# Optimization experiments

Measured on AMD Instinct MI355X. Metric: run time of the kernel, lower is better.

Reference implementation:

```python
import jax, jax.numpy as jnp
import numpy as np

B, D_IN, H, D_OUT, K = 8192, 2048, 2048, 1024, 4
LOGVAR_INIT = -5.0


def setup_inputs() -> dict:
    key = jax.random.key(0)
    ks = jax.random.split(key, 32)
    dims = [(D_IN, H), (H, H), (H, D_OUT)]
    inp = {"x": jax.random.normal(ks[0], (B, D_IN), dtype=jnp.float32)}
    i = 1
    for l, (din, dout) in enumerate(dims):
        inp[f"w_mu{l}"] = 0.1 * jax.random.normal(ks[i], (K, dout, din), dtype=jnp.float32); i += 1
        inp[f"b_mu{l}"] = 0.1 * jax.random.normal(ks[i], (K, dout), dtype=jnp.float32); i += 1
        inp[f"w_lv{l}"] = jnp.full((K,), LOGVAR_INIT, dtype=jnp.float32)
        inp[f"b_lv{l}"] = jnp.full((K,), LOGVAR_INIT, dtype=jnp.float32)
        inp[f"ml{l}"] = jnp.zeros((K,), dtype=jnp.float32)
        # reparameterization noise (randn_like in the torch code), one per component
        inp[f"w_n{l}"] = jax.random.normal(ks[i], (K, dout, din), dtype=jnp.float32); i += 1
        inp[f"b_n{l}"] = jax.random.normal(ks[i], (K, dout), dtype=jnp.float32); i += 1
    return inp


def _mixture_linear(x, w_mu, b_mu, w_lv, b_lv, ml, w_n, b_n):
    # n_components <= n_samples: all K components used, weighted by softmax(mix_logits)
    mix_w = jax.nn.softmax(ml)                               # [K]
    w = w_mu + jnp.exp(0.5 * w_lv)[:, None, None] * w_n      # [K, O, I]
    b = b_mu + jnp.exp(0.5 * b_lv)[:, None] * b_n            # [K, O]
    # sum_k mix_w[k] * (x @ w[k].T + b[k])
    out = jnp.einsum('bi,koi,k->bo', x, w, mix_w)
    out = out + jnp.einsum('k,ko->o', mix_w, b)
    return out


def reference(x,
              w_mu0, b_mu0, w_lv0, b_lv0, ml0, w_n0, b_n0,
              w_mu1, b_mu1, w_lv1, b_lv1, ml1, w_n1, b_n1,
              w_mu2, b_mu2, w_lv2, b_lv2, ml2, w_n2, b_n2):
    h = jax.nn.relu(_mixture_linear(x, w_mu0, b_mu0, w_lv0, b_lv0, ml0, w_n0, b_n0))
    h = jax.nn.relu(_mixture_linear(h, w_mu1, b_mu1, w_lv1, b_lv1, ml1, w_n1, b_n1))
    h = _mixture_linear(h, w_mu2, b_mu2, w_lv2, b_lv2, ml2, w_n2, b_n2)
    return jax.nn.softmax(h, axis=1)
```

## Files before the change

kernel.cpp:

```cpp
#include <hip/hip_runtime.h>
#include <hip/hip_fp16.h>

typedef _Float16 half8 __attribute__((ext_vector_type(8)));
typedef _Float16 half4 __attribute__((ext_vector_type(4)));
typedef float floatx4 __attribute__((ext_vector_type(4)));

#define GLDS16(g, l)                                                           \
  __builtin_amdgcn_global_load_lds(                                            \
      (const __attribute__((address_space(1))) void*)(g),                      \
      (__attribute__((address_space(3))) void*)(l), 16, 0, 0)

__device__ inline void mix_coeffs(const float* lv, const float* ml,
                                  float* cmu, float* cn) {
  float m0 = ml[0], m1 = ml[1], m2 = ml[2], m3 = ml[3];
  float mx = fmaxf(fmaxf(m0, m1), fmaxf(m2, m3));
  float e0 = __expf(m0 - mx), e1 = __expf(m1 - mx);
  float e2 = __expf(m2 - mx), e3 = __expf(m3 - mx);
  float inv = 1.0f / (e0 + e1 + e2 + e3);
  cmu[0] = e0 * inv; cmu[1] = e1 * inv; cmu[2] = e2 * inv; cmu[3] = e3 * inv;
  cn[0] = cmu[0] * __expf(0.5f * lv[0]);
  cn[1] = cmu[1] * __expf(0.5f * lv[1]);
  cn[2] = cmu[2] * __expf(0.5f * lv[2]);
  cn[3] = cmu[3] * __expf(0.5f * lv[3]);
}

__global__ __launch_bounds__(256) void prep_w(
    const float* __restrict__ mu, const float* __restrict__ nz,
    const float* __restrict__ lv, const float* __restrict__ ml,
    _Float16* __restrict__ out, int count) {
  float cmu[4], cn[4];
  mix_coeffs(lv, ml, cmu, cn);
  long i = ((long)blockIdx.x * 256 + threadIdx.x) * 4;
  if (i >= count) return;
  float rx = 0.f, ry = 0.f, rz = 0.f, rw = 0.f;
#pragma unroll
  for (int k = 0; k < 4; ++k) {
    float4 a = *(const float4*)(mu + (long)k * count + i);
    float4 b = *(const float4*)(nz + (long)k * count + i);
    rx += cmu[k] * a.x + cn[k] * b.x;
    ry += cmu[k] * a.y + cn[k] * b.y;
    rz += cmu[k] * a.z + cn[k] * b.z;
    rw += cmu[k] * a.w + cn[k] * b.w;
  }
  half4 h = {(_Float16)rx, (_Float16)ry, (_Float16)rz, (_Float16)rw};
  *(half4*)(out + i) = h;
}

__global__ __launch_bounds__(256) void prep_b(
    const float* __restrict__ bmu, const float* __restrict__ bn,
    const float* __restrict__ lv, const float* __restrict__ ml,
    float* __restrict__ out, int O) {
  float cmu[4], cn[4];
  mix_coeffs(lv, ml, cmu, cn);
  int i = blockIdx.x * 256 + threadIdx.x;
  if (i >= O) return;
  float r = 0.f;
#pragma unroll
  for (int k = 0; k < 4; ++k)
    r += cmu[k] * bmu[k * O + i] + cn[k] * bn[k * O + i];
  out[i] = r;
}

__global__ __launch_bounds__(256) void cvt_half(
    const float* __restrict__ in, _Float16* __restrict__ out) {
  long i = ((long)blockIdx.x * 256 + threadIdx.x) * 4;
  float4 v = *(const float4*)(in + i);
  half4 h = {(_Float16)v.x, (_Float16)v.y, (_Float16)v.z, (_Float16)v.w};
  *(half4*)(out + i) = h;
}

template <bool RELU, bool OUT_HALF>
__global__ __launch_bounds__(256) void gemm_nt(
    const _Float16* __restrict__ A, const _Float16* __restrict__ B,
    const float* __restrict__ bias, void* __restrict__ Cout,
    int M, int N, int K) {
  __shared__ _Float16 sA[128 * 64];
  __shared__ _Float16 sB[128 * 64];

  const int t = threadIdx.x;
  const int l = t & 63;
  const int w = t >> 6;
  const int wr = w >> 1;
  const int wc = w & 1;
  const long rowBlock = (long)blockIdx.x * 128;
  const long colBlock = (long)blockIdx.y * 128;

  floatx4 acc[4][4] = {};

  const _Float16* ga[4];
  const _Float16* gb[4];
#pragma unroll
  for (int j = 0; j < 4; ++j) {
    int p = j * 256 + t;
    int c = p & 7;
    int m = (p >> 3) & 15;
    int mt = p >> 7;
    int gc = c ^ (m & 7);
    ga[j] = A + (rowBlock + mt * 16 + m) * (long)K + gc * 8;
    gb[j] = B + (colBlock + mt * 16 + m) * (long)K + gc * 8;
  }
  char* stA = (char*)sA + w * 1024;
  char* stB = (char*)sB + w * 1024;

  const int mrow = l & 15;
  const int q = l >> 4;
  const int msw = mrow & 7;

  for (int k0 = 0; k0 < K; k0 += 64) {
#pragma unroll
    for (int j = 0; j < 4; ++j) {
      GLDS16(ga[j] + k0, stA + j * 4096);
      GLDS16(gb[j] + k0, stB + j * 4096);
    }
    __syncthreads();
#pragma unroll
    for (int s = 0; s < 2; ++s) {
      const int cidx = (s * 4 + q) ^ msw;
      half8 af[4], bf[4];
#pragma unroll
      for (int r = 0; r < 4; ++r)
        af[r] = *(const half8*)((const char*)sA +
                                ((wr * 4 + r) * 2048 + mrow * 128 + cidx * 16));
#pragma unroll
      for (int c = 0; c < 4; ++c)
        bf[c] = *(const half8*)((const char*)sB +
                                ((wc * 4 + c) * 2048 + mrow * 128 + cidx * 16));
#pragma unroll
      for (int r = 0; r < 4; ++r)
#pragma unroll
        for (int c = 0; c < 4; ++c)
          acc[r][c] = __builtin_amdgcn_mfma_f32_16x16x32_f16(
              af[r], bf[c], acc[r][c], 0, 0, 0);
    }
    __syncthreads();
  }

  const long row0 = rowBlock + wr * 64 + (l >> 4) * 4;
  const long col0 = colBlock + wc * 64 + (l & 15);
  float bv[4];
#pragma unroll
  for (int c = 0; c < 4; ++c) bv[c] = bias[col0 + c * 16];
#pragma unroll
  for (int r = 0; r < 4; ++r) {
#pragma unroll
    for (int c = 0; c < 4; ++c) {
#pragma unroll
      for (int e = 0; e < 4; ++e) {
        float v = acc[r][c][e] + bv[c];
        if (RELU) v = fmaxf(v, 0.0f);
        long row = row0 + r * 16 + e;
        long col = col0 + c * 16;
        if (OUT_HALF)
          ((_Float16*)Cout)[row * N + col] = (_Float16)v;
        else
          ((float*)Cout)[row * N + col] = v;
      }
    }
  }
}

__global__ __launch_bounds__(256) void softmax_rows(float* __restrict__ io) {
  const int N = 1024;
  float* p = io + (long)blockIdx.x * N;
  int t = threadIdx.x;
  int w = t >> 6;
  float4 v = ((const float4*)p)[t];
  float m = fmaxf(fmaxf(v.x, v.y), fmaxf(v.z, v.w));
#pragma unroll
  for (int off = 32; off > 0; off >>= 1) m = fmaxf(m, __shfl_xor(m, off));
  __shared__ float red[8];
  if ((t & 63) == 0) red[w] = m;
  __syncthreads();
  m = fmaxf(fmaxf(red[0], red[1]), fmaxf(red[2], red[3]));
  float4 e;
  e.x = __expf(v.x - m); e.y = __expf(v.y - m);
  e.z = __expf(v.z - m); e.w = __expf(v.w - m);
  float s = e.x + e.y + e.z + e.w;
#pragma unroll
  for (int off = 32; off > 0; off >>= 1) s += __shfl_xor(s, off);
  if ((t & 63) == 0) red[4 + w] = s;
  __syncthreads();
  s = red[4] + red[5] + red[6] + red[7];
  float inv = 1.0f / s;
  float4 o = {e.x * inv, e.y * inv, e.z * inv, e.w * inv};
  ((float4*)p)[t] = o;
}

extern "C" void kernel_launch(void* const* d_in, const int* in_sizes, int n_in,
                              void* d_out, int out_size, void* d_ws,
                              size_t ws_size, hipStream_t stream) {
  const float* x     = (const float*)d_in[0];
  const float* w_mu0 = (const float*)d_in[1];
  const float* b_mu0 = (const float*)d_in[2];
  const float* w_lv0 = (const float*)d_in[3];
  const float* b_lv0 = (const float*)d_in[4];
  const float* ml0   = (const float*)d_in[5];
  const float* w_n0  = (const float*)d_in[6];
  const float* b_n0  = (const float*)d_in[7];
  const float* w_mu1 = (const float*)d_in[8];
  const float* b_mu1 = (const float*)d_in[9];
  const float* w_lv1 = (const float*)d_in[10];
  const float* b_lv1 = (const float*)d_in[11];
  const float* ml1   = (const float*)d_in[12];
  const float* w_n1  = (const float*)d_in[13];
  const float* b_n1  = (const float*)d_in[14];
  const float* w_mu2 = (const float*)d_in[15];
  const float* b_mu2 = (const float*)d_in[16];
  const float* w_lv2 = (const float*)d_in[17];
  const float* b_lv2 = (const float*)d_in[18];
  const float* ml2   = (const float*)d_in[19];
  const float* w_n2  = (const float*)d_in[20];
  const float* b_n2  = (const float*)d_in[21];

  char* ws = (char*)d_ws;
  _Float16* x16 = (_Float16*)(ws);
  _Float16* h0  = (_Float16*)(ws + 33554432);
  _Float16* W0  = (_Float16*)(ws + 67108864);
  _Float16* W1  = (_Float16*)(ws + 75497472);
  _Float16* W2  = (_Float16*)(ws + 83886080);
  float* b0 = (float*)(ws + 88080384);
  float* b1 = (float*)(ws + 88088576);
  float* b2 = (float*)(ws + 88096768);

  prep_w<<<4096, 256, 0, stream>>>(w_mu0, w_n0, w_lv0, ml0, W0, 2048 * 2048);
  prep_w<<<4096, 256, 0, stream>>>(w_mu1, w_n1, w_lv1, ml1, W1, 2048 * 2048);
  prep_w<<<2048, 256, 0, stream>>>(w_mu2, w_n2, w_lv2, ml2, W2, 1024 * 2048);
  prep_b<<<8, 256, 0, stream>>>(b_mu0, b_n0, b_lv0, ml0, b0, 2048);
  prep_b<<<8, 256, 0, stream>>>(b_mu1, b_n1, b_lv1, ml1, b1, 2048);
  prep_b<<<4, 256, 0, stream>>>(b_mu2, b_n2, b_lv2, ml2, b2, 1024);
  cvt_half<<<16384, 256, 0, stream>>>(x, x16);

  gemm_nt<true, true><<<dim3(64, 16), 256, 0, stream>>>(
      x16, W0, b0, h0, 8192, 2048, 2048);
  gemm_nt<true, true><<<dim3(64, 16), 256, 0, stream>>>(
      h0, W1, b1, x16, 8192, 2048, 2048);
  gemm_nt<false, false><<<dim3(64, 8), 256, 0, stream>>>(
      x16, W2, b2, d_out, 8192, 1024, 2048);
  softmax_rows<<<8192, 256, 0, stream>>>((float*)d_out);
}
```

Before: 645.0 us.

## Switch GEMM to 32x32x16 MFMA with wider N tiles and fuse prep kernels

Replaces the 16x16x32 MFMA tiling with 32x32x16 MFMA instructions. The two 2048-wide GEMMs now use 128x256 tiles (CT=4), which halves their grid, and launch_bounds(256,2) is added. The aim is fewer LDS fragment reads per FLOP and more register-level reuse. The seven small prep launches (weight mixing, bias mixing, x conversion) are merged into a single kernel that dispatches on block index, cutting launch overhead. Risks are higher register pressure from the larger accumulators and a less coalesced epilogue store pattern.

Result: faster. 590.7 us (-8.4%).

```diff
diff --git a/kernel.cpp b/kernel.cpp
--- a/kernel.cpp
+++ b/kernel.cpp
@@ -3,7 +3,7 @@
 
 typedef _Float16 half8 __attribute__((ext_vector_type(8)));
 typedef _Float16 half4 __attribute__((ext_vector_type(4)));
-typedef float floatx4 __attribute__((ext_vector_type(4)));
+typedef float floatx16 __attribute__((ext_vector_type(16)));
 
 #define GLDS16(g, l)                                                           \
   __builtin_amdgcn_global_load_lds(                                            \
@@ -24,14 +24,14 @@
   cn[3] = cmu[3] * __expf(0.5f * lv[3]);
 }
 
-__global__ __launch_bounds__(256) void prep_w(
-    const float* __restrict__ mu, const float* __restrict__ nz,
-    const float* __restrict__ lv, const float* __restrict__ ml,
-    _Float16* __restrict__ out, int count) {
+__device__ inline void do_prep_w(const float* __restrict__ mu,
+                                 const float* __restrict__ nz,
+                                 const float* lv, const float* ml,
+                                 _Float16* __restrict__ out, int count,
+                                 int bid) {
   float cmu[4], cn[4];
   mix_coeffs(lv, ml, cmu, cn);
-  long i = ((long)blockIdx.x * 256 + threadIdx.x) * 4;
-  if (i >= count) return;
+  long i = ((long)bid * 256 + threadIdx.x) * 4;
   float rx = 0.f, ry = 0.f, rz = 0.f, rw = 0.f;
 #pragma unroll
   for (int k = 0; k < 4; ++k) {
@@ -46,13 +46,13 @@
   *(half4*)(out + i) = h;
 }
 
-__global__ __launch_bounds__(256) void prep_b(
-    const float* __restrict__ bmu, const float* __restrict__ bn,
-    const float* __restrict__ lv, const float* __restrict__ ml,
-    float* __restrict__ out, int O) {
+__device__ inline void do_prep_b(const float* __restrict__ bmu,
+                                 const float* __restrict__ bn,
+                                 const float* lv, const float* ml,
+                                 float* __restrict__ out, int O, int bid) {
   float cmu[4], cn[4];
   mix_coeffs(lv, ml, cmu, cn);
-  int i = blockIdx.x * 256 + threadIdx.x;
+  int i = bid * 256 + threadIdx.x;
   if (i >= O) return;
   float r = 0.f;
 #pragma unroll
@@ -61,21 +61,49 @@
   out[i] = r;
 }
 
-__global__ __launch_bounds__(256) void cvt_half(
-    const float* __restrict__ in, _Float16* __restrict__ out) {
-  long i = ((long)blockIdx.x * 256 + threadIdx.x) * 4;
+__device__ inline void do_cvt(const float* __restrict__ in,
+                              _Float16* __restrict__ out, int bid) {
+  long i = ((long)bid * 256 + threadIdx.x) * 4;
   float4 v = *(const float4*)(in + i);
   half4 h = {(_Float16)v.x, (_Float16)v.y, (_Float16)v.z, (_Float16)v.w};
   *(half4*)(out + i) = h;
 }
 
-template <bool RELU, bool OUT_HALF>
-__global__ __launch_bounds__(256) void gemm_nt(
+struct PrepArgs {
+  const float* x; _Float16* x16;
+  const float* wmu0; const float* wn0; const float* wlv0; const float* ml0; _Float16* W0;
+  const float* wmu1; const float* wn1; const float* wlv1; const float* ml1; _Float16* W1;
+  const float* wmu2; const float* wn2; const float* wlv2; const float* ml2; _Float16* W2;
+  const float* bmu0; const float* bn0; const float* blv0; float* b0;
+  const float* bmu1; const float* bn1; const float* blv1; float* b1;
+  const float* bmu2; const float* bn2; const float* blv2; float* b2;
+};
+
+__global__ __launch_bounds__(256) void prep_all(PrepArgs a) {
+  int b = blockIdx.x;
+  if (b < 16384) { do_cvt(a.x, a.x16, b); return; }
+  b -= 16384;
+  if (b < 4096) { do_prep_w(a.wmu0, a.wn0, a.wlv0, a.ml0, a.W0, 2048 * 2048, b); return; }
+  b -= 4096;
+  if (b < 4096) { do_prep_w(a.wmu1, a.wn1, a.wlv1, a.ml1, a.W1, 2048 * 2048, b); return; }
+  b -= 4096;
+  if (b < 2048) { do_prep_w(a.wmu2, a.wn2, a.wlv2, a.ml2, a.W2, 1024 * 2048, b); return; }
+  b -= 2048;
+  if (b < 8) { do_prep_b(a.bmu0, a.bn0, a.blv0, a.ml0, a.b0, 2048, b); return; }
+  b -= 8;
+  if (b < 8) { do_prep_b(a.bmu1, a.bn1, a.blv1, a.ml1, a.b1, 2048, b); return; }
+  b -= 8;
+  do_prep_b(a.bmu2, a.bn2, a.blv2, a.ml2, a.b2, 1024, b);
+}
+
+template <int CT, bool RELU, bool OUT_HALF>
+__global__ __launch_bounds__(256, 2) void gemm_nt(
     const _Float16* __restrict__ A, const _Float16* __restrict__ B,
     const float* __restrict__ bias, void* __restrict__ Cout,
     int M, int N, int K) {
+  constexpr int BN = CT * 64;
   __shared__ _Float16 sA[128 * 64];
-  __shared__ _Float16 sB[128 * 64];
+  __shared__ _Float16 sB[BN * 64];
 
   const int t = threadIdx.x;
   const int l = t & 63;
@@ -83,77 +111,79 @@
   const int wr = w >> 1;
   const int wc = w & 1;
   const long rowBlock = (long)blockIdx.x * 128;
-  const long colBlock = (long)blockIdx.y * 128;
-
-  floatx4 acc[4][4] = {};
+  const long colBlock = (long)blockIdx.y * BN;
+
+  floatx16 acc[2][CT] = {};
 
   const _Float16* ga[4];
-  const _Float16* gb[4];
+  const _Float16* gb[2 * CT];
 #pragma unroll
   for (int j = 0; j < 4; ++j) {
     int p = j * 256 + t;
-    int c = p & 7;
-    int m = (p >> 3) & 15;
-    int mt = p >> 7;
-    int gc = c ^ (m & 7);
-    ga[j] = A + (rowBlock + mt * 16 + m) * (long)K + gc * 8;
-    gb[j] = B + (colBlock + mt * 16 + m) * (long)K + gc * 8;
+    int r = p >> 3, pos = p & 7;
+    int gc = pos ^ (r & 7);
+    ga[j] = A + (rowBlock + r) * (long)K + gc * 8;
+  }
+#pragma unroll
+  for (int j = 0; j < 2 * CT; ++j) {
+    int p = j * 256 + t;
+    int r = p >> 3, pos = p & 7;
+    int gc = pos ^ (r & 7);
+    gb[j] = B + (colBlock + r) * (long)K + gc * 8;
   }
   char* stA = (char*)sA + w * 1024;
   char* stB = (char*)sB + w * 1024;
 
-  const int mrow = l & 15;
-  const int q = l >> 4;
-  const int msw = mrow & 7;
+  const int rm = l & 31;
+  const int kh = l >> 5;
+  const int sw = rm & 7;
 
   for (int k0 = 0; k0 < K; k0 += 64) {
 #pragma unroll
-    for (int j = 0; j < 4; ++j) {
-      GLDS16(ga[j] + k0, stA + j * 4096);
-      GLDS16(gb[j] + k0, stB + j * 4096);
+    for (int j = 0; j < 4; ++j) GLDS16(ga[j] + k0, stA + j * 4096);
+#pragma unroll
+    for (int j = 0; j < 2 * CT; ++j) GLDS16(gb[j] + k0, stB + j * 4096);
+    __syncthreads();
+#pragma unroll
+    for (int s = 0; s < 4; ++s) {
+      const int pos = (s * 2 + kh) ^ sw;
+      half8 af[2], bf[CT];
+#pragma unroll
+      for (int rt = 0; rt < 2; ++rt)
+        af[rt] = *(const half8*)((const char*)sA +
+                                 ((wr * 64 + rt * 32 + rm) * 128 + pos * 16));
+#pragma unroll
+      for (int ct = 0; ct < CT; ++ct)
+        bf[ct] = *(const half8*)((const char*)sB +
+                                 ((wc * (CT * 32) + ct * 32 + rm) * 128 + pos * 16));
+#pragma unroll
+      for (int rt = 0; rt < 2; ++rt)
+#pragma unroll
+        for (int ct = 0; ct < CT; ++ct)
+          acc[rt][ct] = __builtin_amdgcn_mfma_f32_32x32x16_f16(
+              af[rt], bf[ct], acc[rt][ct], 0, 0, 0);
     }
     __syncthreads();
-#pragma unroll
-    for (int s = 0; s < 2; ++s) {
-      const int cidx = (s * 4 + q) ^ msw;
-      half8 af[4], bf[4];
-#pragma unroll
-      for (int r = 0; r < 4; ++r)
-        af[r] = *(const half8*)((const char*)sA +
-                                ((wr * 4 + r) * 2048 + mrow * 128 + cidx * 16));
-#pragma unroll
-      for (int c = 0; c < 4; ++c)
-        bf[c] = *(const half8*)((const char*)sB +
-                                ((wc * 4 + c) * 2048 + mrow * 128 + cidx * 16));
-#pragma unroll
-      for (int r = 0; r < 4; ++r)
-#pragma unroll
-        for (int c = 0; c < 4; ++c)
-          acc[r][c] = __builtin_amdgcn_mfma_f32_16x16x32_f16(
-              af[r], bf[c], acc[r][c], 0, 0, 0);
-    }
-    __syncthreads();
-  }
-
-  const long row0 = rowBlock + wr * 64 + (l >> 4) * 4;
-  const long col0 = colBlock + wc * 64 + (l & 15);
-  float bv[4];
-#pragma unroll
-  for (int c = 0; c < 4; ++c) bv[c] = bias[col0 + c * 16];
-#pragma unroll
-  for (int r = 0; r < 4; ++r) {
-#pragma unroll
-    for (int c = 0; c < 4; ++c) {
-#pragma unroll
-      for (int e = 0; e < 4; ++e) {
-        float v = acc[r][c][e] + bv[c];
+  }
+
+  const int cl = l & 31;
+  const int rh = (l >> 5) * 4;
+#pragma unroll
+  for (int rt = 0; rt < 2; ++rt) {
+#pragma unroll
+    for (int ct = 0; ct < CT; ++ct) {
+      const long colg = colBlock + wc * (CT * 32) + ct * 32 + cl;
+      const float bv = bias[colg];
+#pragma unroll
+      for (int reg = 0; reg < 16; ++reg) {
+        const int rowin = (reg & 3) + 8 * (reg >> 2) + rh;
+        const long rowg = rowBlock + wr * 64 + rt * 32 + rowin;
+        float v = acc[rt][ct][reg] + bv;
         if (RELU) v = fmaxf(v, 0.0f);
-        long row = row0 + r * 16 + e;
-        long col = col0 + c * 16;
         if (OUT_HALF)
-          ((_Float16*)Cout)[row * N + col] = (_Float16)v;
+          ((_Float16*)Cout)[rowg * N + colg] = (_Float16)v;
         else
-          ((float*)Cout)[row * N + col] = v;
+          ((float*)Cout)[rowg * N + colg] = v;
       }
     }
   }
@@ -189,29 +219,6 @@
 extern "C" void kernel_launch(void* const* d_in, const int* in_sizes, int n_in,
                               void* d_out, int out_size, void* d_ws,
                               size_t ws_size, hipStream_t stream) {
-  const float* x     = (const float*)d_in[0];
-  const float* w_mu0 = (const float*)d_in[1];
-  const float* b_mu0 = (const float*)d_in[2];
-  const float* w_lv0 = (const float*)d_in[3];
-  const float* b_lv0 = (const float*)d_in[4];
-  const float* ml0   = (const float*)d_in[5];
-  const float* w_n0  = (const float*)d_in[6];
-  const float* b_n0  = (const float*)d_in[7];
-  const float* w_mu1 = (const float*)d_in[8];
-  const float* b_mu1 = (const float*)d_in[9];
-  const float* w_lv1 = (const float*)d_in[10];
-  const float* b_lv1 = (const float*)d_in[11];
-  const float* ml1   = (const float*)d_in[12];
-  const float* w_n1  = (const float*)d_in[13];
-  const float* b_n1  = (const float*)d_in[14];
-  const float* w_mu2 = (const float*)d_in[15];
-  const float* b_mu2 = (const float*)d_in[16];
-  const float* w_lv2 = (const float*)d_in[17];
-  const float* b_lv2 = (const float*)d_in[18];
-  const float* ml2   = (const float*)d_in[19];
-  const float* w_n2  = (const float*)d_in[20];
-  const float* b_n2  = (const float*)d_in[21];
-
   char* ws = (char*)d_ws;
   _Float16* x16 = (_Float16*)(ws);
   _Float16* h0  = (_Float16*)(ws + 33554432);
@@ -222,19 +229,29 @@
   float* b1 = (float*)(ws + 88088576);
   float* b2 = (float*)(ws + 88096768);
 
-  prep_w<<<4096, 256, 0, stream>>>(w_mu0, w_n0, w_lv0, ml0, W0, 2048 * 2048);
-  prep_w<<<4096, 256, 0, stream>>>(w_mu1, w_n1, w_lv1, ml1, W1, 2048 * 2048);
-  prep_w<<<2048, 256, 0, stream>>>(w_mu2, w_n2, w_lv2, ml2, W2, 1024 * 2048);
-  prep_b<<<8, 256, 0, stream>>>(b_mu0, b_n0, b_lv0, ml0, b0, 2048);
-  prep_b<<<8, 256, 0, stream>>>(b_mu1, b_n1, b_lv1, ml1, b1, 2048);
-  prep_b<<<4, 256, 0, stream>>>(b_mu2, b_n2, b_lv2, ml2, b2, 1024);
-  cvt_half<<<16384, 256, 0, stream>>>(x, x16);
-
-  gemm_nt<true, true><<<dim3(64, 16), 256, 0, stream>>>(
+  PrepArgs a;
+  a.x = (const float*)d_in[0]; a.x16 = x16;
+  a.wmu0 = (const float*)d_in[1];  a.bmu0 = (const float*)d_in[2];
+  a.wlv0 = (const float*)d_in[3];  a.blv0 = (const float*)d_in[4];
+  a.ml0  = (const float*)d_in[5];
+  a.wn0  = (const float*)d_in[6];  a.bn0  = (const float*)d_in[7];
+  a.wmu1 = (const float*)d_in[8];  a.bmu1 = (const float*)d_in[9];
+  a.wlv1 = (const float*)d_in[10]; a.blv1 = (const float*)d_in[11];
+  a.ml1  = (const float*)d_in[12];
+  a.wn1  = (const float*)d_in[13]; a.bn1  = (const float*)d_in[14];
+  a.wmu2 = (const float*)d_in[15]; a.bmu2 = (const float*)d_in[16];
+  a.wlv2 = (const float*)d_in[17]; a.blv2 = (const float*)d_in[18];
+  a.ml2  = (const float*)d_in[19];
+  a.wn2  = (const float*)d_in[20]; a.bn2  = (const float*)d_in[21];
+  a.W0 = W0; a.W1 = W1; a.W2 = W2; a.b0 = b0; a.b1 = b1; a.b2 = b2;
+
+  prep_all<<<26644, 256, 0, stream>>>(a);
+
+  gemm_nt<4, true, true><<<dim3(64, 8), 256, 0, stream>>>(
       x16, W0, b0, h0, 8192, 2048, 2048);
-  gemm_nt<true, true><<<dim3(64, 16), 256, 0, stream>>>(
+  gemm_nt<4, true, true><<<dim3(64, 8), 256, 0, stream>>>(
       h0, W1, b1, x16, 8192, 2048, 2048);
-  gemm_nt<false, false><<<dim3(64, 8), 256, 0, stream>>>(
+  gemm_nt<2, false, false><<<dim3(64, 8), 256, 0, stream>>>(
       x16, W2, b2, d_out, 8192, 1024, 2048);
   softmax_rows<<<8192, 256, 0, stream>>>((float*)d_out);
 }
```
